# Kernel optimization log

Measured on AMD Instinct MI355X. Metric: run time of the kernel, lower is better.

The kernel has to match this reference:

```python
import jax, jax.numpy as jnp
import numpy as np

N_HEADS = 8
N_GROUPS = 32  # GroupNorm groups (normalization(channels) in guided-diffusion)
EPS = 1e-5


def setup_inputs() -> dict:
    key = jax.random.key(0)
    ks = jax.random.split(key, 7)
    b, c, hh, ww = 16, 512, 32, 32
    x = jax.random.normal(ks[0], (b, c, hh, ww), dtype=jnp.float32)
    norm_w = 1.0 + 0.02 * jax.random.normal(ks[1], (c,), dtype=jnp.float32)
    norm_b = 0.02 * jax.random.normal(ks[2], (c,), dtype=jnp.float32)
    # pointwise Conv1d == matmul over channels; note proj_out is zero-initialized
    # in the original, we use random weights so the op is non-trivial.
    qkv_w = jax.random.normal(ks[3], (3 * c, c), dtype=jnp.float32) / np.sqrt(c).astype(np.float32)
    qkv_b = 0.02 * jax.random.normal(ks[4], (3 * c,), dtype=jnp.float32)
    proj_w = jax.random.normal(ks[5], (c, c), dtype=jnp.float32) / np.sqrt(c).astype(np.float32)
    proj_b = 0.02 * jax.random.normal(ks[6], (c,), dtype=jnp.float32)
    return {"x": x, "norm_w": norm_w, "norm_b": norm_b,
            "qkv_w": qkv_w, "qkv_b": qkv_b, "proj_w": proj_w, "proj_b": proj_b}


def reference(x, norm_w, norm_b, qkv_w, qkv_b, proj_w, proj_b):
    b, c, hh, ww = x.shape
    t = hh * ww
    xf = x.reshape(b, c, t)

    # GroupNorm(32, c): normalize over (c//G channels, T) per group
    xg = xf.reshape(b, N_GROUPS, (c // N_GROUPS) * t)
    mu = jnp.mean(xg, axis=-1, keepdims=True)
    var = jnp.var(xg, axis=-1, keepdims=True)
    hn = ((xg - mu) * jax.lax.rsqrt(var + EPS)).reshape(b, c, t)
    hn = hn * norm_w[:, None] + norm_b[:, None]

    # pointwise conv: [b, 3c, t]
    qkv = jnp.einsum('oc,bct->bot', qkv_w, hn) + qkv_b[:, None]

    ch = c // N_HEADS
    qkv = qkv.reshape(b * N_HEADS, 3 * ch, t)
    q, k, v = jnp.split(qkv, 3, axis=1)  # each [b*H, ch, t]
    scale = np.float32(1.0 / np.sqrt(np.sqrt(ch)))
    w = jnp.einsum('bct,bcs->bts', q * scale, k * scale)  # [b*H, t, t]
    w = jax.nn.softmax(w.astype(jnp.float32), axis=-1).astype(qkv.dtype)
    a = jnp.einsum('bts,bcs->bct', w, v).reshape(b, c, t)

    h = jnp.einsum('oc,bct->bot', proj_w, a) + proj_b[:, None]
    return (xf + h).reshape(b, c, hh, ww)
```

## Files before the change

### kernel.cpp

```cpp
#include <hip/hip_runtime.h>

#define TPB 256

typedef __attribute__((ext_vector_type(8))) __bf16 bf16x8;
typedef __attribute__((ext_vector_type(4))) float f32x4;
typedef __attribute__((ext_vector_type(8))) unsigned short u16x8;
typedef __attribute__((ext_vector_type(4))) unsigned short u16x4;
typedef __attribute__((ext_vector_type(4))) unsigned int u32x4;
typedef __attribute__((ext_vector_type(2))) unsigned int u32x2;

typedef __attribute__((address_space(1))) const void gconst_void;
typedef __attribute__((address_space(3))) void lds_void;

__device__ __forceinline__ unsigned short f2bf(float f) {
  unsigned u = __builtin_bit_cast(unsigned, f);
  u += 0x7FFFu + ((u >> 16) & 1u);
  return (unsigned short)(u >> 16);
}

__device__ __forceinline__ float exp2_fast(float x) {
  float r;
  asm("v_exp_f32 %0, %1" : "=v"(r) : "v"(x));
  return r;
}

__device__ __forceinline__ float rcp_fast(float x) {
  float r;
  asm("v_rcp_f32 %0, %1" : "=v"(r) : "v"(x));
  return r;
}

__device__ __forceinline__ unsigned cvt_pk_bf16(float lo, float hi) {
  unsigned r;
  asm("v_cvt_pk_bf16_f32 %0, %1, %2" : "=v"(r) : "v"(lo), "v"(hi));
  return r;
}


__global__ __launch_bounds__(256) void k_gn_fused(const float* __restrict__ x,
                                                  const float* __restrict__ nw,
                                                  const float* __restrict__ nb,
                                                  unsigned short* __restrict__ hnT) {
  int bg = blockIdx.x;
  int b = bg >> 5, g = bg & 31;
  size_t base = (size_t)(b * 512 + g * 16) * 1024;
  const float4* p = reinterpret_cast<const float4*>(x + base);
  float s = 0.f, ss = 0.f;
#pragma unroll
  for (int i = 0; i < 16; ++i) {
    float4 v = p[threadIdx.x + i * 256];
    s += v.x + v.y + v.z + v.w;
    ss += v.x * v.x + v.y * v.y + v.z * v.z + v.w * v.w;
  }
#pragma unroll
  for (int off = 1; off < 64; off <<= 1) {
    s += __shfl_xor(s, off, 64);
    ss += __shfl_xor(ss, off, 64);
  }
  __shared__ float rbuf[4][2];
  __shared__ float stat[2];
  int wave = threadIdx.x >> 6;
  if ((threadIdx.x & 63) == 0) { rbuf[wave][0] = s; rbuf[wave][1] = ss; }
  __syncthreads();
  if (threadIdx.x == 0) {
    float S = 0.f, SS = 0.f;
    for (int i = 0; i < 4; ++i) { S += rbuf[i][0]; SS += rbuf[i][1]; }
    float m = S * (1.f / 16384.f);
    float var = SS * (1.f / 16384.f) - m * m;
    stat[0] = m;
    stat[1] = rsqrtf(var + 1e-5f);
  }
  __syncthreads();
  float mu = stat[0], rinv = stat[1];

  int tid = threadIdx.x;
#pragma unroll
  for (int q = 0; q < 2; ++q) {
    int c0 = g * 16 + q * 8;
    float a[8], bb[8];
#pragma unroll
    for (int cc = 0; cc < 8; ++cc) {
      a[cc] = rinv * nw[c0 + cc];
      bb[cc] = nb[c0 + cc] - mu * a[cc];
    }
    size_t cpart = (size_t)(c0 >> 5) * 512 + (size_t)((c0 >> 3) & 3) * 128;
#pragma unroll
    for (int it = 0; it < 4; ++it) {
      int t = it * 256 + tid;
      u16x8 o;
#pragma unroll
      for (int cc = 0; cc < 8; ++cc) {
        float v = x[base + (size_t)(q * 8 + cc) * 1024 + t];
        o[cc] = f2bf(v * a[cc] + bb[cc]);
      }
      size_t dst = (size_t)b * 524288 + (size_t)(t >> 4) * 8192 + cpart + (t & 15) * 8;
      *reinterpret_cast<u16x8*>(hnT + dst) = o;
    }
  }
}

__global__ void k_prep_w(const float* __restrict__ qkv_w, const float* __restrict__ proj_w,
                         unsigned short* __restrict__ wqb, unsigned short* __restrict__ wpb) {
  int i = blockIdx.x * blockDim.x + threadIdx.x;
  if (i < 98304) {
    int r = i >> 6, k8 = i & 63;
    const float4* s = reinterpret_cast<const float4*>(qkv_w + (size_t)r * 512 + k8 * 8);
    float4 v0 = s[0], v1 = s[1];
    u16x8 o;
    o[0] = f2bf(v0.x); o[1] = f2bf(v0.y); o[2] = f2bf(v0.z); o[3] = f2bf(v0.w);
    o[4] = f2bf(v1.x); o[5] = f2bf(v1.y); o[6] = f2bf(v1.z); o[7] = f2bf(v1.w);
    size_t d = (size_t)(r >> 4) * 8192 + (size_t)(k8 >> 2) * 512 + (k8 & 3) * 128 + (r & 15) * 8;
    *reinterpret_cast<u16x8*>(wqb + d) = o;
  } else {
    int j = i - 98304;
    float4 v = reinterpret_cast<const float4*>(proj_w)[j];
    u16x4 o;
    o[0] = f2bf(v.x); o[1] = f2bf(v.y); o[2] = f2bf(v.z); o[3] = f2bf(v.w);
    reinterpret_cast<u16x4*>(wpb)[j] = o;
  }
}

#define MFMAS(AF, BF)                                                                     \
  do {                                                                                    \
    _Pragma("unroll") for (int mi = 0; mi < 4; ++mi)                                      \
      _Pragma("unroll") for (int ni = 0; ni < 4; ++ni)                                    \
        acc[mi][ni] =                                                                     \
            __builtin_amdgcn_mfma_f32_16x16x32_bf16(AF[mi], BF[ni], acc[mi][ni], 0, 0, 0);\
  } while (0)

#define LOADT(DA, DB, kb)                                                                 \
  do {                                                                                    \
    _Pragma("unroll") for (int mi = 0; mi < 4; ++mi)                                      \
      DA[mi] = *reinterpret_cast<const bf16x8*>(pA + (size_t)mi * 8192 + (kb) * 512);     \
    _Pragma("unroll") for (int ni = 0; ni < 4; ++ni)                                      \
      DB[ni] = *reinterpret_cast<const bf16x8*>(pB + (size_t)ni * 8192 + (kb) * 512);     \
  } while (0)

__global__ __launch_bounds__(256, 1) void k_qkv_gemm(
    const unsigned short* __restrict__ hnT, const unsigned short* __restrict__ wq,
    const float* __restrict__ qkv_b, unsigned short* __restrict__ Q,
    unsigned short* __restrict__ Kq, unsigned short* __restrict__ Vq) {
  int tid = threadIdx.x;
  int lane = tid & 63, wave = tid >> 6;
  int wm = wave >> 1, wn = wave & 1;
  int g = lane >> 4, li = lane & 15;

  int wg = blockIdx.x;
  int lin = (wg & 7) * 192 + (wg >> 3);
  int bx = lin % 12;
  int tmp = lin / 12;
  int by = tmp & 7;
  int b = tmp >> 3;
  int mbase = by * 128;
  int nbase = bx * 128;

  const unsigned short* pA =
      hnT + (size_t)b * 524288 + (size_t)((mbase + wm * 64) >> 4) * 8192 + lane * 8;
  const unsigned short* pB = wq + (size_t)((nbase + wn * 64) >> 4) * 8192 + lane * 8;

  f32x4 zero = {0.f, 0.f, 0.f, 0.f};
  f32x4 acc[4][4];
#pragma unroll
  for (int mi = 0; mi < 4; ++mi)
#pragma unroll
    for (int ni = 0; ni < 4; ++ni) acc[mi][ni] = zero;

  bf16x8 a0[4], b0[4], a1[4], b1[4];
  LOADT(a0, b0, 0);
#pragma unroll
  for (int kb = 0; kb < 16; kb += 2) {
    if (kb + 1 < 16) LOADT(a1, b1, kb + 1);
    MFMAS(a0, b0);
    if (kb + 2 < 16) LOADT(a0, b0, kb + 2);
    MFMAS(a1, b1);
  }

  const float SCALE = 0.42466090143f;
#pragma unroll
  for (int ni = 0; ni < 4; ++ni) {
    int o = nbase + wn * 64 + ni * 16 + li;
    int h = o / 192;
    int j = o - h * 192;
    int bh = b * 8 + h;
    float bias = qkv_b[o];
#pragma unroll
    for (int mi = 0; mi < 4; ++mi) {
      int t0 = mbase + wm * 64 + mi * 16 + g * 4;
      f32x4 v = acc[mi][ni];
      if (j < 64) {
#pragma unroll
        for (int r = 0; r < 4; ++r)
          Q[((size_t)bh * 1024 + t0 + r) * 64 + j] = f2bf((v[r] + bias) * SCALE);
      } else if (j < 128) {
#pragma unroll
        for (int r = 0; r < 4; ++r)
          Kq[((size_t)bh * 1024 + t0 + r) * 64 + (j - 64)] = f2bf((v[r] + bias) * SCALE);
      } else {
        int ch = j - 128;
        int nj = ch >> 4, liv = ch & 15;
        int stile = t0 >> 6, s0 = t0 & 63;
        int kkc = s0 >> 5, gk = (s0 >> 3) & 3, e0 = s0 & 7;
        u16x4 pv;
#pragma unroll
        for (int r = 0; r < 4; ++r) pv[r] = f2bf(v[r] + bias);
        *reinterpret_cast<u16x4*>(Vq + (size_t)bh * 65536 + (size_t)stile * 4096 +
                                  nj * 1024 + kkc * 512 + gk * 128 + liv * 8 + e0) = pv;
      }
    }
  }
}

__global__ __launch_bounds__(256) void k_attn(
    const unsigned short* __restrict__ Q, const unsigned short* __restrict__ K,
    const unsigned short* __restrict__ Vp, unsigned short* __restrict__ aT) {
  __shared__ unsigned short Kls[2][8192];
  int tid = threadIdx.x;
  int lane = tid & 63, w = tid >> 6;
  int g = lane >> 4, li = lane & 15;

  int wg = blockIdx.x;
  int lin = (wg & 7) * 128 + (wg >> 3);
  int qt = lin & 7;
  int bh = lin >> 3;
  int tq0 = qt * 128;
  int b = bh >> 3, h = bh & 7;

  const unsigned short* Kg = K + (size_t)bh * 1024 * 64;
  const unsigned short* Vb = Vp + (size_t)bh * 65536 + lane * 8;

  bf16x8 qf[2][2];
#pragma unroll
  for (int qi = 0; qi < 2; ++qi) {
    int t = tq0 + w * 32 + qi * 16 + li;
    const unsigned short* qp = Q + ((size_t)bh * 1024 + t) * 64 + g * 8;
    qf[qi][0] = *reinterpret_cast<const bf16x8*>(qp);
    qf[qi][1] = *reinterpret_cast<const bf16x8*>(qp + 32);
  }

  const unsigned short* kg[4];
#pragma unroll
  for (int i = 0; i < 4; ++i) {
    int r = w * 32 + i * 8 + (lane >> 3);
    int hh = (r ^ (r >> 2)) & 7;
    int c = ((lane & 7) ^ hh) * 8;
    kg[i] = Kg + (size_t)r * 64 + c;
  }

  int srowK = ((li >> 2) << 3) | (li & 3);

  f32x4 zero = {0.f, 0.f, 0.f, 0.f};
  f32x4 oacc[2][4];
  f32x4 l_acc[2];
#pragma unroll
  for (int qi = 0; qi < 2; ++qi) {
    l_acc[qi] = zero;
#pragma unroll
    for (int nj = 0; nj < 4; ++nj) oacc[qi][nj] = zero;
  }
  u32x4 onesw = {0x3F803F80u, 0x3F803F80u, 0x3F803F80u, 0x3F803F80u};
  bf16x8 ones = __builtin_bit_cast(bf16x8, onesw);

#define ISSUE(pp, ph)                                                                    \
  do {                                                                                   \
    _Pragma("unroll") for (int i = 0; i < 4; ++i)                                        \
        __builtin_amdgcn_global_load_lds((gconst_void*)(kg[i] + (size_t)(ph) * 8192),    \
                                         (lds_void*)&Kls[pp][w * 2048 + i * 512], 16, 0, \
                                         0);                                             \
  } while (0)

  ISSUE(0, 0);
  for (int ph = 0; ph < 8; ++ph) {
    asm volatile("s_waitcnt vmcnt(0) lgkmcnt(0)" ::: "memory");
    __builtin_amdgcn_s_barrier();
    asm volatile("" ::: "memory");
    if (ph < 7) ISSUE((ph + 1) & 1, ph + 1);

#pragma unroll
    for (int st = 0; st < 2; ++st) {
      const unsigned short* kbase = &Kls[ph & 1][st * 4096];
      const unsigned short* vt = Vb + (size_t)(ph * 2 + st) * 4096;

      bf16x8 vf0[4];
#pragma unroll
      for (int i = 0; i < 4; ++i) vf0[i] = *reinterpret_cast<const bf16x8*>(vt + i * 512);

      f32x4 sacc[2][4];
      __builtin_amdgcn_s_setprio(1);
#pragma unroll
      for (int ni = 0; ni < 4; ++ni) {
        int rK = ((ni >> 1) << 5) + ((ni & 1) << 2) + srowK;
        int hs = ((rK ^ (rK >> 2)) & 7) << 4;
        int off0 = ((g << 4)) ^ hs;
        int off1 = (64 + (g << 4)) ^ hs;
        bf16x8 kf0 = *reinterpret_cast<const bf16x8*>(&kbase[rK * 64 + (off0 >> 1)]);
        bf16x8 kf1 = *reinterpret_cast<const bf16x8*>(&kbase[rK * 64 + (off1 >> 1)]);
#pragma unroll
        for (int qi = 0; qi < 2; ++qi) {
          f32x4 s0 = __builtin_amdgcn_mfma_f32_16x16x32_bf16(kf0, qf[qi][0], zero, 0, 0, 0);
          sacc[qi][ni] = __builtin_amdgcn_mfma_f32_16x16x32_bf16(kf1, qf[qi][1], s0, 0, 0, 0);
        }
      }
      __builtin_amdgcn_s_setprio(0);

      bf16x8 pfrag[2][2];
#pragma unroll
      for (int qi = 0; qi < 2; ++qi) {
#pragma unroll
        for (int ni = 0; ni < 4; ++ni)
#pragma unroll
          for (int r = 0; r < 4; ++r) sacc[qi][ni][r] = exp2_fast(sacc[qi][ni][r]);
#pragma unroll
        for (int kk = 0; kk < 2; ++kk) {
          u32x4 pw;
          pw[0] = cvt_pk_bf16(sacc[qi][2 * kk][0], sacc[qi][2 * kk][1]);
          pw[1] = cvt_pk_bf16(sacc[qi][2 * kk][2], sacc[qi][2 * kk][3]);
          pw[2] = cvt_pk_bf16(sacc[qi][2 * kk + 1][0], sacc[qi][2 * kk + 1][1]);
          pw[3] = cvt_pk_bf16(sacc[qi][2 * kk + 1][2], sacc[qi][2 * kk + 1][3]);
          pfrag[qi][kk] = __builtin_bit_cast(bf16x8, pw);
        }
        l_acc[qi] = __builtin_amdgcn_mfma_f32_16x16x32_bf16(ones, pfrag[qi][0], l_acc[qi], 0, 0, 0);
        l_acc[qi] = __builtin_amdgcn_mfma_f32_16x16x32_bf16(ones, pfrag[qi][1], l_acc[qi], 0, 0, 0);
      }

      bf16x8 vf1[4];
#pragma unroll
      for (int i = 0; i < 4; ++i)
        vf1[i] = *reinterpret_cast<const bf16x8*>(vt + (4 + i) * 512);

      __builtin_amdgcn_s_setprio(1);
#pragma unroll
      for (int nj = 0; nj < 2; ++nj)
#pragma unroll
        for (int qi = 0; qi < 2; ++qi) {
          oacc[qi][nj] = __builtin_amdgcn_mfma_f32_16x16x32_bf16(vf0[nj * 2 + 0], pfrag[qi][0], oacc[qi][nj], 0, 0, 0);
          oacc[qi][nj] = __builtin_amdgcn_mfma_f32_16x16x32_bf16(vf0[nj * 2 + 1], pfrag[qi][1], oacc[qi][nj], 0, 0, 0);
        }
#pragma unroll
      for (int nj = 2; nj < 4; ++nj)
#pragma unroll
        for (int qi = 0; qi < 2; ++qi) {
          oacc[qi][nj] = __builtin_amdgcn_mfma_f32_16x16x32_bf16(vf1[(nj - 2) * 2 + 0], pfrag[qi][0], oacc[qi][nj], 0, 0, 0);
          oacc[qi][nj] = __builtin_amdgcn_mfma_f32_16x16x32_bf16(vf1[(nj - 2) * 2 + 1], pfrag[qi][1], oacc[qi][nj], 0, 0, 0);
        }
      __builtin_amdgcn_s_setprio(0);
    }
  }
#undef ISSUE

#pragma unroll
  for (int qi = 0; qi < 2; ++qi) {
    float inv = rcp_fast(l_acc[qi][0]);
    int t = tq0 + w * 32 + qi * 16 + li;
#pragma unroll
    for (int nj = 0; nj < 4; ++nj) {
      u32x2 ov;
      ov[0] = cvt_pk_bf16(oacc[qi][nj][0] * inv, oacc[qi][nj][1] * inv);
      ov[1] = cvt_pk_bf16(oacc[qi][nj][2] * inv, oacc[qi][nj][3] * inv);
      *reinterpret_cast<u32x2*>(aT + ((size_t)b * 1024 + t) * 512 + h * 64 + nj * 16 + g * 4) = ov;
    }
  }
}

__global__ __launch_bounds__(256) void k_proj_gemm(
    const unsigned short* __restrict__ aT, const unsigned short* __restrict__ wp,
    const float* __restrict__ proj_b, const float* __restrict__ x,
    float* __restrict__ out) {
  __shared__ unsigned short As[2][4096];
  __shared__ unsigned short Bs[2][4096];
  int tid = threadIdx.x;
  int lane = tid & 63, wave = tid >> 6;
  int wm = wave >> 1, wn = wave & 1;
  int g = lane >> 4, li = lane & 15;

  int wg = blockIdx.x;
  int lin = (wg & 7) * 64 + (wg >> 3);
  int bx = lin & 7;
  int tmp = lin >> 3;
  int by = tmp & 3;
  int b = tmp >> 2;
  int mbase = by * 128;
  int nbase = bx * 128;

  const unsigned short* Ag = wp + (size_t)mbase * 512;
  const unsigned short* Bg = aT + (size_t)b * 1024 * 512 + (size_t)nbase * 512;

  int kq = (lane & 3) ^ ((lane >> 3) & 3);
  int rst = wave * 32 + (lane >> 2);
  const char* pA0 = (const char*)Ag + (size_t)rst * 1024 + kq * 16;
  const char* pA1 = pA0 + 16 * 1024;
  const char* pB0 = (const char*)Bg + (size_t)rst * 1024 + kq * 16;
  const char* pB1 = pB0 + 16 * 1024;
  int ldsA0 = wave * 1024, ldsA1 = wave * 1024 + 512;

  int voff = 32 * li + 8 * (g ^ ((li >> 1) & 3));

  f32x4 zero = {0.f, 0.f, 0.f, 0.f};
  f32x4 acc[4][4];
#pragma unroll
  for (int mi = 0; mi < 4; ++mi)
#pragma unroll
    for (int ni = 0; ni < 4; ++ni) acc[mi][ni] = zero;

#define GISSUE(k0, buf)                                                                  \
  do {                                                                                   \
    __builtin_amdgcn_global_load_lds((gconst_void*)(pA0 + (k0) * 2),                     \
                                     (lds_void*)&As[buf][ldsA0], 16, 0, 0);              \
    __builtin_amdgcn_global_load_lds((gconst_void*)(pA1 + (k0) * 2),                     \
                                     (lds_void*)&As[buf][ldsA1], 16, 0, 0);              \
    __builtin_amdgcn_global_load_lds((gconst_void*)(pB0 + (k0) * 2),                     \
                                     (lds_void*)&Bs[buf][ldsA0], 16, 0, 0);              \
    __builtin_amdgcn_global_load_lds((gconst_void*)(pB1 + (k0) * 2),                     \
                                     (lds_void*)&Bs[buf][ldsA1], 16, 0, 0);              \
  } while (0)

  GISSUE(0, 0);
#pragma unroll
  for (int kk = 0; kk < 16; ++kk) {
    asm volatile("s_waitcnt vmcnt(0)" ::: "memory");
    __builtin_amdgcn_s_barrier();
    asm volatile("" ::: "memory");
    if (kk < 15) GISSUE((kk + 1) * 32, (kk + 1) & 1);
    const int cur = kk & 1;
    bf16x8 af[4], bfr[4];
#pragma unroll
    for (int mi = 0; mi < 4; ++mi)
      af[mi] = *reinterpret_cast<const bf16x8*>(&As[cur][wm * 2048 + mi * 512 + voff]);
#pragma unroll
    for (int ni = 0; ni < 4; ++ni)
      bfr[ni] = *reinterpret_cast<const bf16x8*>(&Bs[cur][wn * 2048 + ni * 512 + voff]);
#pragma unroll
    for (int mi = 0; mi < 4; ++mi)
#pragma unroll
      for (int ni = 0; ni < 4; ++ni)
        acc[mi][ni] = __builtin_amdgcn_mfma_f32_16x16x32_bf16(af[mi], bfr[ni], acc[mi][ni], 0, 0, 0);
  }
#undef GISSUE

#pragma unroll
  for (int mi = 0; mi < 4; ++mi) {
#pragma unroll
    for (int ni = 0; ni < 4; ++ni) {
      int t = nbase + wn * 64 + ni * 16 + li;
      f32x4 v = acc[mi][ni];
#pragma unroll
      for (int r = 0; r < 4; ++r) {
        int o = mbase + wm * 64 + mi * 16 + g * 4 + r;
        size_t idx = ((size_t)(b * 512 + o)) * 1024 + t;
        out[idx] = v[r] + proj_b[o] + x[idx];
      }
    }
  }
}

extern "C" void kernel_launch(void* const* d_in, const int* in_sizes, int n_in,
                              void* d_out, int out_size, void* d_ws, size_t ws_size,
                              hipStream_t stream) {
  (void)in_sizes; (void)n_in; (void)out_size; (void)ws_size;
  const float* x = (const float*)d_in[0];
  const float* norm_w = (const float*)d_in[1];
  const float* norm_b = (const float*)d_in[2];
  const float* qkv_w = (const float*)d_in[3];
  const float* qkv_b = (const float*)d_in[4];
  const float* proj_w = (const float*)d_in[5];
  const float* proj_b = (const float*)d_in[6];
  float* out = (float*)d_out;

  char* ws = (char*)d_ws;
  size_t off = 0;
  unsigned short* hnT = (unsigned short*)(ws + off); off += (size_t)16 * 1024 * 512 * 2;
  unsigned short* wqb = (unsigned short*)(ws + off); off += (size_t)1536 * 512 * 2;
  unsigned short* wpb = (unsigned short*)(ws + off); off += (size_t)512 * 512 * 2;
  unsigned short* Qb = (unsigned short*)(ws + off); off += (size_t)128 * 1024 * 64 * 2;
  unsigned short* Kb = (unsigned short*)(ws + off); off += (size_t)128 * 1024 * 64 * 2;
  unsigned short* Vb = (unsigned short*)(ws + off); off += (size_t)128 * 1024 * 64 * 2;

  k_gn_fused<<<512, TPB, 0, stream>>>(x, norm_w, norm_b, hnT);
  k_prep_w<<<640, TPB, 0, stream>>>(qkv_w, proj_w, wqb, wpb);
  k_qkv_gemm<<<1536, TPB, 0, stream>>>(hnT, wqb, qkv_b, Qb, Kb, Vb);
  k_attn<<<1024, TPB, 0, stream>>>(Qb, Kb, Vb, hnT );
  k_proj_gemm<<<512, TPB, 0, stream>>>(hnT, wpb, proj_b, x, out);
}
```

Before: 124.9 us.

## Process 256 queries per attention block to reuse K/V tiles

```diff
diff --git a/kernel.cpp b/kernel.cpp
--- a/kernel.cpp
+++ b/kernel.cpp
@@ -219,22 +219,22 @@
   int g = lane >> 4, li = lane & 15;
 
   int wg = blockIdx.x;
-  int lin = (wg & 7) * 128 + (wg >> 3);
-  int qt = lin & 7;
-  int bh = lin >> 3;
-  int tq0 = qt * 128;
+  int lin = (wg & 7) * 64 + (wg >> 3);
+  int qp = lin & 3;
+  int bh = lin >> 2;
+  int tq0 = qp * 256;
   int b = bh >> 3, h = bh & 7;
 
   const unsigned short* Kg = K + (size_t)bh * 1024 * 64;
   const unsigned short* Vb = Vp + (size_t)bh * 65536 + lane * 8;
 
-  bf16x8 qf[2][2];
-#pragma unroll
-  for (int qi = 0; qi < 2; ++qi) {
-    int t = tq0 + w * 32 + qi * 16 + li;
-    const unsigned short* qp = Q + ((size_t)bh * 1024 + t) * 64 + g * 8;
-    qf[qi][0] = *reinterpret_cast<const bf16x8*>(qp);
-    qf[qi][1] = *reinterpret_cast<const bf16x8*>(qp + 32);
+  bf16x8 qf[4][2];
+#pragma unroll
+  for (int qi = 0; qi < 4; ++qi) {
+    int t = tq0 + (qi >> 1) * 128 + w * 32 + (qi & 1) * 16 + li;
+    const unsigned short* qp_ = Q + ((size_t)bh * 1024 + t) * 64 + g * 8;
+    qf[qi][0] = *reinterpret_cast<const bf16x8*>(qp_);
+    qf[qi][1] = *reinterpret_cast<const bf16x8*>(qp_ + 32);
   }
 
   const unsigned short* kg[4];
@@ -249,10 +249,10 @@
   int srowK = ((li >> 2) << 3) | (li & 3);
 
   f32x4 zero = {0.f, 0.f, 0.f, 0.f};
-  f32x4 oacc[2][4];
-  f32x4 l_acc[2];
-#pragma unroll
-  for (int qi = 0; qi < 2; ++qi) {
+  f32x4 oacc[4][4];
+  f32x4 l_acc[4];
+#pragma unroll
+  for (int qi = 0; qi < 4; ++qi) {
     l_acc[qi] = zero;
 #pragma unroll
     for (int nj = 0; nj < 4; ++nj) oacc[qi][nj] = zero;
@@ -268,6 +268,43 @@
                                          0);                                             \
   } while (0)
 
+#define QK2(q0, sacc)                                                                    \
+  do {                                                                                   \
+    _Pragma("unroll") for (int ni = 0; ni < 4; ++ni) {                                   \
+      int rK = ((ni >> 1) << 5) + ((ni & 1) << 2) + srowK;                               \
+      int hs = ((rK ^ (rK >> 2)) & 7) << 4;                                              \
+      int off0 = (g << 4) ^ hs;                                                          \
+      int off1 = (64 + (g << 4)) ^ hs;                                                   \
+      bf16x8 kf0 = *reinterpret_cast<const bf16x8*>(&kbase[rK * 64 + (off0 >> 1)]);      \
+      bf16x8 kf1 = *reinterpret_cast<const bf16x8*>(&kbase[rK * 64 + (off1 >> 1)]);      \
+      _Pragma("unroll") for (int u = 0; u < 2; ++u) {                                    \
+        f32x4 s0 = __builtin_amdgcn_mfma_f32_16x16x32_bf16(kf0, qf[(q0) + u][0], zero, 0, 0, 0); \
+        sacc[u][ni] = __builtin_amdgcn_mfma_f32_16x16x32_bf16(kf1, qf[(q0) + u][1], s0, 0, 0, 0); \
+      }                                                                                  \
+    }                                                                                    \
+  } while (0)
+
+#define SM2(q0, sacc)                                                                    \
+  do {                                                                                   \
+    _Pragma("unroll") for (int u = 0; u < 2; ++u) {                                      \
+      _Pragma("unroll") for (int ni = 0; ni < 4; ++ni)                                   \
+        _Pragma("unroll") for (int r = 0; r < 4; ++r)                                    \
+            sacc[u][ni][r] = exp2_fast(sacc[u][ni][r]);                                  \
+      _Pragma("unroll") for (int kk = 0; kk < 2; ++kk) {                                 \
+        u32x4 pw;                                                                        \
+        pw[0] = cvt_pk_bf16(sacc[u][2 * kk][0], sacc[u][2 * kk][1]);                     \
+        pw[1] = cvt_pk_bf16(sacc[u][2 * kk][2], sacc[u][2 * kk][3]);                     \
+        pw[2] = cvt_pk_bf16(sacc[u][2 * kk + 1][0], sacc[u][2 * kk + 1][1]);             \
+        pw[3] = cvt_pk_bf16(sacc[u][2 * kk + 1][2], sacc[u][2 * kk + 1][3]);             \
+        pfrag[(q0) + u][kk] = __builtin_bit_cast(bf16x8, pw);                            \
+      }                                                                                  \
+      l_acc[(q0) + u] = __builtin_amdgcn_mfma_f32_16x16x32_bf16(ones, pfrag[(q0) + u][0],\
+                                                                l_acc[(q0) + u], 0, 0, 0);\
+      l_acc[(q0) + u] = __builtin_amdgcn_mfma_f32_16x16x32_bf16(ones, pfrag[(q0) + u][1],\
+                                                                l_acc[(q0) + u], 0, 0, 0);\
+    }                                                                                    \
+  } while (0)
+
   ISSUE(0, 0);
   for (int ph = 0; ph < 8; ++ph) {
     asm volatile("s_waitcnt vmcnt(0) lgkmcnt(0)" ::: "memory");
@@ -280,46 +317,25 @@
       const unsigned short* kbase = &Kls[ph & 1][st * 4096];
       const unsigned short* vt = Vb + (size_t)(ph * 2 + st) * 4096;
 
+      bf16x8 pfrag[4][2];
+
       bf16x8 vf0[4];
 #pragma unroll
       for (int i = 0; i < 4; ++i) vf0[i] = *reinterpret_cast<const bf16x8*>(vt + i * 512);
 
-      f32x4 sacc[2][4];
-      __builtin_amdgcn_s_setprio(1);
-#pragma unroll
-      for (int ni = 0; ni < 4; ++ni) {
-        int rK = ((ni >> 1) << 5) + ((ni & 1) << 2) + srowK;
-        int hs = ((rK ^ (rK >> 2)) & 7) << 4;
-        int off0 = ((g << 4)) ^ hs;
-        int off1 = (64 + (g << 4)) ^ hs;
-        bf16x8 kf0 = *reinterpret_cast<const bf16x8*>(&kbase[rK * 64 + (off0 >> 1)]);
-        bf16x8 kf1 = *reinterpret_cast<const bf16x8*>(&kbase[rK * 64 + (off1 >> 1)]);
-#pragma unroll
-        for (int qi = 0; qi < 2; ++qi) {
-          f32x4 s0 = __builtin_amdgcn_mfma_f32_16x16x32_bf16(kf0, qf[qi][0], zero, 0, 0, 0);
-          sacc[qi][ni] = __builtin_amdgcn_mfma_f32_16x16x32_bf16(kf1, qf[qi][1], s0, 0, 0, 0);
-        }
+      {
+        f32x4 sacc[2][4];
+        __builtin_amdgcn_s_setprio(1);
+        QK2(0, sacc);
+        __builtin_amdgcn_s_setprio(0);
+        SM2(0, sacc);
       }
-      __builtin_amdgcn_s_setprio(0);
-
-      bf16x8 pfrag[2][2];
-#pragma unroll
-      for (int qi = 0; qi < 2; ++qi) {
-#pragma unroll
-        for (int ni = 0; ni < 4; ++ni)
-#pragma unroll
-          for (int r = 0; r < 4; ++r) sacc[qi][ni][r] = exp2_fast(sacc[qi][ni][r]);
-#pragma unroll
-        for (int kk = 0; kk < 2; ++kk) {
-          u32x4 pw;
-          pw[0] = cvt_pk_bf16(sacc[qi][2 * kk][0], sacc[qi][2 * kk][1]);
-          pw[1] = cvt_pk_bf16(sacc[qi][2 * kk][2], sacc[qi][2 * kk][3]);
-          pw[2] = cvt_pk_bf16(sacc[qi][2 * kk + 1][0], sacc[qi][2 * kk + 1][1]);
-          pw[3] = cvt_pk_bf16(sacc[qi][2 * kk + 1][2], sacc[qi][2 * kk + 1][3]);
-          pfrag[qi][kk] = __builtin_bit_cast(bf16x8, pw);
-        }
-        l_acc[qi] = __builtin_amdgcn_mfma_f32_16x16x32_bf16(ones, pfrag[qi][0], l_acc[qi], 0, 0, 0);
-        l_acc[qi] = __builtin_amdgcn_mfma_f32_16x16x32_bf16(ones, pfrag[qi][1], l_acc[qi], 0, 0, 0);
+      {
+        f32x4 sacc[2][4];
+        __builtin_amdgcn_s_setprio(1);
+        QK2(2, sacc);
+        __builtin_amdgcn_s_setprio(0);
+        SM2(2, sacc);
       }
 
       bf16x8 vf1[4];
@@ -331,14 +347,14 @@
 #pragma unroll
       for (int nj = 0; nj < 2; ++nj)
 #pragma unroll
-        for (int qi = 0; qi < 2; ++qi) {
+        for (int qi = 0; qi < 4; ++qi) {
           oacc[qi][nj] = __builtin_amdgcn_mfma_f32_16x16x32_bf16(vf0[nj * 2 + 0], pfrag[qi][0], oacc[qi][nj], 0, 0, 0);
           oacc[qi][nj] = __builtin_amdgcn_mfma_f32_16x16x32_bf16(vf0[nj * 2 + 1], pfrag[qi][1], oacc[qi][nj], 0, 0, 0);
         }
 #pragma unroll
       for (int nj = 2; nj < 4; ++nj)
 #pragma unroll
-        for (int qi = 0; qi < 2; ++qi) {
+        for (int qi = 0; qi < 4; ++qi) {
           oacc[qi][nj] = __builtin_amdgcn_mfma_f32_16x16x32_bf16(vf1[(nj - 2) * 2 + 0], pfrag[qi][0], oacc[qi][nj], 0, 0, 0);
           oacc[qi][nj] = __builtin_amdgcn_mfma_f32_16x16x32_bf16(vf1[(nj - 2) * 2 + 1], pfrag[qi][1], oacc[qi][nj], 0, 0, 0);
         }
@@ -346,11 +362,13 @@
     }
   }
 #undef ISSUE
-
-#pragma unroll
-  for (int qi = 0; qi < 2; ++qi) {
+#undef QK2
+#undef SM2
+
+#pragma unroll
+  for (int qi = 0; qi < 4; ++qi) {
     float inv = rcp_fast(l_acc[qi][0]);
-    int t = tq0 + w * 32 + qi * 16 + li;
+    int t = tq0 + (qi >> 1) * 128 + w * 32 + (qi & 1) * 16 + li;
 #pragma unroll
     for (int nj = 0; nj < 4; ++nj) {
       u32x2 ov;
@@ -477,6 +495,6 @@
   k_gn_fused<<<512, TPB, 0, stream>>>(x, norm_w, norm_b, hnT);
   k_prep_w<<<640, TPB, 0, stream>>>(qkv_w, proj_w, wqb, wpb);
   k_qkv_gemm<<<1536, TPB, 0, stream>>>(hnT, wqb, qkv_b, Qb, Kb, Vb);
-  k_attn<<<1024, TPB, 0, stream>>>(Qb, Kb, Vb, hnT );
+  k_attn<<<512, TPB, 0, stream>>>(Qb, Kb, Vb, hnT );
   k_proj_gemm<<<512, TPB, 0, stream>>>(hnT, wpb, proj_b, x, out);
 }
```

Result: slower. 135.8 us (+8.7%).
